# Performance work log

Hardware: AMD Instinct MI355X
Metric: run time of the kernel (lower is better)

## Reference

```python
import jax, jax.numpy as jnp
import numpy as np

# Model dims from __init__(k_mix=4, h_size=16)
H = 128            # GRU units = h_size * 8
F = 8              # per-step input features (reshape [-1,1,1,8])
KMIX = 4           # K = max(2, k_mix)
OUT = KMIX * 3     # 12; dense outputs K*3*8 = 96, reshaped to [8, 12]
T = 262144         # number of sequential bottom_generator steps


def setup_inputs() -> dict:
    key = jax.random.key(0)
    k0, k1, k2, k3 = jax.random.split(key, 4)
    even_x = jax.random.normal(k0, (T, 1, 1, F), dtype=jnp.float32)
    # GRU params (Keras layout: kernel [F, 3H], recurrent_kernel [H, 3H],
    # bias [2, 3H] for reset_after=True; gate order z, r, h)
    gru_kernel = jax.random.normal(k1, (F, 3 * H), dtype=jnp.float32) / np.float32(np.sqrt(F))
    gru_rec_kernel = jax.random.normal(k2, (H, 3 * H), dtype=jnp.float32) / np.float32(np.sqrt(H))
    gru_bias = jnp.zeros((2, 3 * H), dtype=jnp.float32)
    dense_kernel = jax.random.normal(k3, (H, F * OUT), dtype=jnp.float32) / np.float32(np.sqrt(H))
    dense_bias = jnp.zeros((F * OUT,), dtype=jnp.float32)
    return {
        "even_x": even_x,
        "gru_kernel": gru_kernel,
        "gru_rec_kernel": gru_rec_kernel,
        "gru_bias": gru_bias,
        "dense_kernel": dense_kernel,
        "dense_bias": dense_bias,
    }


def _bottom_params(even_x, gru_kernel, gru_rec_kernel, gru_bias, dense_kernel, dense_bias):
    # bottom_x = reshape(even_x, [-1, 1, 1, 8]); shift right by one with zeros
    x = even_x.reshape(-1, F)                                  # [T, 8]
    x = jnp.concatenate([jnp.zeros((1, F), x.dtype), x[:-1]], axis=0)
    b_i = gru_bias[0]
    b_r = gru_bias[1]
    # Precompute input projections for all steps (batchable part)
    gx_all = x @ gru_kernel + b_i                              # [T, 3H]

    def step(h, gx):
        gh = h @ gru_rec_kernel + b_r                          # [3H]
        xz, xr, xh = jnp.split(gx, 3)
        hz, hr, hn = jnp.split(gh, 3)
        z = jax.nn.sigmoid(xz + hz)
        r = jax.nn.sigmoid(xr + hr)
        hh = jnp.tanh(xh + r * hn)                             # reset_after=True
        h_new = z * h + (1.0 - z) * hh                         # Keras GRU update
        return h_new, h_new

    h0 = jnp.zeros((H,), x.dtype)
    _, hs = jax.lax.scan(step, h0, gx_all)                     # [T, H]
    y = hs @ dense_kernel + dense_bias                         # [T, 96]
    return y.reshape(-1, F, OUT)                               # [T, 8, 12]


def reference(even_x, gru_kernel, gru_rec_kernel, gru_bias, dense_kernel, dense_bias):
    return _bottom_params(even_x, gru_kernel, gru_rec_kernel, gru_bias,
                          dense_kernel, dense_bias)
```

## Files before the change

### kernel.cpp

```cpp
#include <hip/hip_runtime.h>
#include <hip/hip_bf16.h>
#include <stdint.h>
#include <stddef.h>

#define T_STEPS 262144
#define CHUNK   64
#define NCHUNK  (T_STEPS / CHUNK)

typedef float v2f __attribute__((ext_vector_type(2)));
typedef float v4f __attribute__((ext_vector_type(4)));

#define PKFMA(acc, a, b) \
    asm("v_pk_fma_f32 %0, %1, %2, %0" : "+v"(acc) : "v"(a), "v"(b))

__device__ __forceinline__ float dpp_xor1(float x) {
    int y = __builtin_amdgcn_mov_dpp(__builtin_bit_cast(int, x), 0xB1, 0xF, 0xF, true);
    return __builtin_bit_cast(float, y);
}
__device__ __forceinline__ float dpp_xor2(float x) {
    int y = __builtin_amdgcn_mov_dpp(__builtin_bit_cast(int, x), 0x4E, 0xF, 0xF, true);
    return __builtin_bit_cast(float, y);
}

#define FOR16(M) M(0) M(1) M(2) M(3) M(4) M(5) M(6) M(7) \
                 M(8) M(9) M(10) M(11) M(12) M(13) M(14) M(15)

__global__ __launch_bounds__(512) void gru_scan(
    const float* __restrict__ xg,
    const float* __restrict__ gk,
    const float* __restrict__ gr,
    const float* __restrict__ gb,
    __hip_bfloat16* __restrict__ hsT)
{
    const int tid = threadIdx.x;
    const int col = tid >> 2;
    const int q   = tid & 3;
    const int rq  = q << 5;

    __shared__ float hbuf[2][4][132];
    __shared__ float xsh[2][512];

#define DECLW(p) v2f wz##p, wr##p, wn##p;
    FOR16(DECLW)
#undef DECLW
#define LOADW(p) { const int r = rq + 2 * (p); \
    wz##p.x = gr[r * 384 + col];        wz##p.y = gr[(r + 1) * 384 + col]; \
    wr##p.x = gr[r * 384 + 128 + col];  wr##p.y = gr[(r + 1) * 384 + 128 + col]; \
    wn##p.x = gr[r * 384 + 256 + col];  wn##p.y = gr[(r + 1) * 384 + 256 + col]; }
    FOR16(LOADW)
#undef LOADW

    v2f kz, kr, kn;
    {
        const int f = q << 1;
        kz.x = gk[f * 384 + col];        kz.y = gk[(f + 1) * 384 + col];
        kr.x = gk[f * 384 + 128 + col];  kr.y = gk[(f + 1) * 384 + 128 + col];
        kn.x = gk[f * 384 + 256 + col];  kn.y = gk[(f + 1) * 384 + 256 + col];
    }
    const float bz  = gb[col]       + gb[384 + col];
    const float brc = gb[128 + col] + gb[512 + col];
    const float bin = gb[256 + col];
    const float brn = gb[640 + col];

    if (tid < 128) {
        hbuf[0][0][tid] = 0.0f; hbuf[0][1][tid] = 0.0f;
        hbuf[0][2][tid] = 0.0f; hbuf[0][3][tid] = 0.0f;
    }
    float hprev = 0.0f;
    float px = (tid >= 8) ? xg[tid - 8] : 0.0f;
    __syncthreads();

    for (int c = 0; c < NCHUNK; ++c) {
        const int cb = c & 1;
        xsh[cb][tid] = px;
        if (c + 1 < NCHUNK) px = xg[(c + 1) * 512 - 8 + tid];
        asm volatile("s_waitcnt lgkmcnt(0)" ::: "memory");
        __builtin_amdgcn_s_barrier();

#pragma unroll 1
        for (int s = 0; s < CHUNK; ++s) {
            const int t  = (c << 6) + s;
            const int rb = s & 1;
            const v4f* hq = (const v4f*)&hbuf[rb][q][rq];

            v2f az0 = {0.f, 0.f}, az1 = {0.f, 0.f};
            v2f ar0 = {0.f, 0.f}, ar1 = {0.f, 0.f};
            v2f an0 = {0.f, 0.f}, an1 = {0.f, 0.f};

#define QROW(m, pa, pb) { const v4f h4 = hq[m]; \
    const v2f ha = __builtin_shufflevector(h4, h4, 0, 1); \
    const v2f hb = __builtin_shufflevector(h4, h4, 2, 3); \
    PKFMA(az0, ha, wz##pa); PKFMA(az1, hb, wz##pb); \
    PKFMA(ar0, ha, wr##pa); PKFMA(ar1, hb, wr##pb); \
    PKFMA(an0, ha, wn##pa); PKFMA(an1, hb, wn##pb); }
            QROW(0, 0, 1)  QROW(1, 2, 3)   QROW(2, 4, 5)   QROW(3, 6, 7)
            QROW(4, 8, 9)  QROW(5, 10, 11) QROW(6, 12, 13) QROW(7, 14, 15)
#undef QROW

            const v2f xv = *(const v2f*)&xsh[cb][(s << 3) + (q << 1)];
            PKFMA(az0, xv, kz);
            PKFMA(ar0, xv, kr);
            v2f gx = {0.f, 0.f};
            PKFMA(gx, xv, kn);

            const v2f azs = az0 + az1;
            const v2f ars = ar0 + ar1;
            const v2f ans = an0 + an1;
            float pz  = azs.x + azs.y;
            float pr  = ars.x + ars.y;
            float pn  = ans.x + ans.y;
            float pxn = gx.x + gx.y;
            pz  += dpp_xor1(pz);  pz  += dpp_xor2(pz);
            pr  += dpp_xor1(pr);  pr  += dpp_xor2(pr);
            pn  += dpp_xor1(pn);  pn  += dpp_xor2(pn);
            pxn += dpp_xor1(pxn); pxn += dpp_xor2(pxn);

            const float zarg = pz + bz;
            const float rarg = pr + brc;
            const float hn   = pn + brn;
            const float xh   = pxn + bin;
            const float z  = 1.0f / (1.0f + __expf(-zarg));
            const float rg = 1.0f / (1.0f + __expf(-rarg));
            const float hh = 1.0f - 2.0f / (1.0f + __expf(2.0f * fmaf(rg, hn, xh)));
            const float hnew = fmaf(z, hprev - hh, hh);
            hprev = hnew;

            hbuf[rb ^ 1][q][col] = hnew;
            if (q == 1) {
                hsT[(size_t)col * T_STEPS + t] = __float2bfloat16(hnew);
            }
            asm volatile("s_waitcnt lgkmcnt(0)" ::: "memory");
            __builtin_amdgcn_s_barrier();
        }
    }
}

__global__ __launch_bounds__(256) void dense_out(
    const __hip_bfloat16* __restrict__ hsT,
    const float* __restrict__ dk,
    const float* __restrict__ db,
    float* __restrict__ out)
{
    __shared__ float wl[128 * 96];
    for (int k = threadIdx.x; k < 128 * 96; k += 256) wl[k] = dk[k];
    __syncthreads();

    const int t = blockIdx.x * 256 + threadIdx.x;
    v4f acc[24];
#pragma unroll
    for (int o = 0; o < 24; ++o) acc[o] = ((const v4f*)db)[o];

#pragma unroll 4
    for (int i = 0; i < 128; ++i) {
        const float h = __bfloat162float(hsT[(size_t)i * T_STEPS + t]);
        const v4f* wp = (const v4f*)&wl[i * 96];
#pragma unroll
        for (int o = 0; o < 24; ++o) {
            const v4f wv = wp[o];
            acc[o].x = fmaf(h, wv.x, acc[o].x);
            acc[o].y = fmaf(h, wv.y, acc[o].y);
            acc[o].z = fmaf(h, wv.z, acc[o].z);
            acc[o].w = fmaf(h, wv.w, acc[o].w);
        }
    }
    v4f* op = (v4f*)(out + (size_t)t * 96);
#pragma unroll
    for (int o = 0; o < 24; ++o) op[o] = acc[o];
}

extern "C" void kernel_launch(void* const* d_in, const int* in_sizes, int n_in,
                              void* d_out, int out_size, void* d_ws, size_t ws_size,
                              hipStream_t stream) {
    const float* even_x = (const float*)d_in[0];
    const float* gk     = (const float*)d_in[1];
    const float* gr     = (const float*)d_in[2];
    const float* gb     = (const float*)d_in[3];
    const float* dk     = (const float*)d_in[4];
    const float* db     = (const float*)d_in[5];
    float* out          = (float*)d_out;

    const size_t need = (size_t)128 * T_STEPS * sizeof(__hip_bfloat16);
    __hip_bfloat16* hsT = (ws_size >= need) ? (__hip_bfloat16*)d_ws
                                            : (__hip_bfloat16*)d_out;

    gru_scan<<<1, 512, 0, stream>>>(even_x, gk, gr, gb, hsT);
    dense_out<<<T_STEPS / 256, 256, 0, stream>>>(hsT, dk, db, out);
}
```

Before: 165.8 ms.

## Stage hidden states in LDS per chunk, use native exp2/rcp, compiler FMAs

Instead of 128 scattered 2-byte global stores per step, hidden states are kept in an LDS history buffer and written once per 64-step chunk as coalesced 16-byte vector stores. Sigmoid and tanh now use the hardware exp2 and rcp builtins instead of __expf plus a full-precision divide. The inline-asm packed FMAs are replaced with elementwise fma builtins that use one accumulator chain instead of two. Launch bounds also gain a min-blocks hint. The single accumulator makes the dependency chain longer, and the approximate rcp may cost some accuracy.

```diff
diff --git a/kernel.cpp b/kernel.cpp
--- a/kernel.cpp
+++ b/kernel.cpp
@@ -6,12 +6,11 @@
 #define T_STEPS 262144
 #define CHUNK   64
 #define NCHUNK  (T_STEPS / CHUNK)
+#define LOG2E   1.442695041f
 
 typedef float v2f __attribute__((ext_vector_type(2)));
 typedef float v4f __attribute__((ext_vector_type(4)));
-
-#define PKFMA(acc, a, b) \
-    asm("v_pk_fma_f32 %0, %1, %2, %0" : "+v"(acc) : "v"(a), "v"(b))
+typedef unsigned int v4u __attribute__((ext_vector_type(4)));
 
 __device__ __forceinline__ float dpp_xor1(float x) {
     int y = __builtin_amdgcn_mov_dpp(__builtin_bit_cast(int, x), 0xB1, 0xF, 0xF, true);
@@ -22,10 +21,13 @@
     return __builtin_bit_cast(float, y);
 }
 
+__device__ __forceinline__ float rcpf_(float x)  { return __builtin_amdgcn_rcpf(x); }
+__device__ __forceinline__ float exp2f_(float x) { return __builtin_amdgcn_exp2f(x); }
+
 #define FOR16(M) M(0) M(1) M(2) M(3) M(4) M(5) M(6) M(7) \
                  M(8) M(9) M(10) M(11) M(12) M(13) M(14) M(15)
 
-__global__ __launch_bounds__(512) void gru_scan(
+__global__ __launch_bounds__(512, 2) void gru_scan(
     const float* __restrict__ xg,
     const float* __restrict__ gk,
     const float* __restrict__ gr,
@@ -39,6 +41,7 @@
 
     __shared__ float hbuf[2][4][132];
     __shared__ float xsh[2][512];
+    __shared__ __hip_bfloat16 hist[CHUNK][128];
 
 #define DECLW(p) v2f wz##p, wr##p, wn##p;
     FOR16(DECLW)
@@ -79,36 +82,33 @@
 
 #pragma unroll 1
         for (int s = 0; s < CHUNK; ++s) {
-            const int t  = (c << 6) + s;
             const int rb = s & 1;
             const v4f* hq = (const v4f*)&hbuf[rb][q][rq];
 
-            v2f az0 = {0.f, 0.f}, az1 = {0.f, 0.f};
-            v2f ar0 = {0.f, 0.f}, ar1 = {0.f, 0.f};
-            v2f an0 = {0.f, 0.f}, an1 = {0.f, 0.f};
+            v2f az = {0.f, 0.f}, ar = {0.f, 0.f}, an = {0.f, 0.f};
 
 #define QROW(m, pa, pb) { const v4f h4 = hq[m]; \
     const v2f ha = __builtin_shufflevector(h4, h4, 0, 1); \
     const v2f hb = __builtin_shufflevector(h4, h4, 2, 3); \
-    PKFMA(az0, ha, wz##pa); PKFMA(az1, hb, wz##pb); \
-    PKFMA(ar0, ha, wr##pa); PKFMA(ar1, hb, wr##pb); \
-    PKFMA(an0, ha, wn##pa); PKFMA(an1, hb, wn##pb); }
+    az = __builtin_elementwise_fma(ha, wz##pa, az); \
+    az = __builtin_elementwise_fma(hb, wz##pb, az); \
+    ar = __builtin_elementwise_fma(ha, wr##pa, ar); \
+    ar = __builtin_elementwise_fma(hb, wr##pb, ar); \
+    an = __builtin_elementwise_fma(ha, wn##pa, an); \
+    an = __builtin_elementwise_fma(hb, wn##pb, an); }
             QROW(0, 0, 1)  QROW(1, 2, 3)   QROW(2, 4, 5)   QROW(3, 6, 7)
             QROW(4, 8, 9)  QROW(5, 10, 11) QROW(6, 12, 13) QROW(7, 14, 15)
 #undef QROW
 
             const v2f xv = *(const v2f*)&xsh[cb][(s << 3) + (q << 1)];
-            PKFMA(az0, xv, kz);
-            PKFMA(ar0, xv, kr);
+            az = __builtin_elementwise_fma(xv, kz, az);
+            ar = __builtin_elementwise_fma(xv, kr, ar);
             v2f gx = {0.f, 0.f};
-            PKFMA(gx, xv, kn);
-
-            const v2f azs = az0 + az1;
-            const v2f ars = ar0 + ar1;
-            const v2f ans = an0 + an1;
-            float pz  = azs.x + azs.y;
-            float pr  = ars.x + ars.y;
-            float pn  = ans.x + ans.y;
+            gx = __builtin_elementwise_fma(xv, kn, gx);
+
+            float pz  = az.x + az.y;
+            float pr  = ar.x + ar.y;
+            float pn  = an.x + an.y;
             float pxn = gx.x + gx.y;
             pz  += dpp_xor1(pz);  pz  += dpp_xor2(pz);
             pr  += dpp_xor1(pr);  pr  += dpp_xor2(pr);
@@ -119,18 +119,37 @@
             const float rarg = pr + brc;
             const float hn   = pn + brn;
             const float xh   = pxn + bin;
-            const float z  = 1.0f / (1.0f + __expf(-zarg));
-            const float rg = 1.0f / (1.0f + __expf(-rarg));
-            const float hh = 1.0f - 2.0f / (1.0f + __expf(2.0f * fmaf(rg, hn, xh)));
+            const float z  = rcpf_(1.0f + exp2f_(-LOG2E * zarg));
+            const float rg = rcpf_(1.0f + exp2f_(-LOG2E * rarg));
+            const float a2 = fmaf(rg, hn, xh);
+            const float hh = fmaf(-2.0f, rcpf_(1.0f + exp2f_(2.0f * LOG2E * a2)), 1.0f);
             const float hnew = fmaf(z, hprev - hh, hh);
             hprev = hnew;
 
             hbuf[rb ^ 1][q][col] = hnew;
-            if (q == 1) {
-                hsT[(size_t)col * T_STEPS + t] = __float2bfloat16(hnew);
-            }
+            if (q == 1) hist[s][col] = __float2bfloat16(hnew);
             asm volatile("s_waitcnt lgkmcnt(0)" ::: "memory");
             __builtin_amdgcn_s_barrier();
+        }
+
+        {
+            const int fc   = tid >> 2;
+            const int part = tid & 3;
+            const int sb   = part << 4;
+            unsigned int d[8];
+#pragma unroll
+            for (int j = 0; j < 8; ++j) {
+                const unsigned int lo =
+                    __builtin_bit_cast(unsigned short, hist[sb + 2 * j][fc]);
+                const unsigned int hi =
+                    __builtin_bit_cast(unsigned short, hist[sb + 2 * j + 1][fc]);
+                d[j] = lo | (hi << 16);
+            }
+            v4u* dst = (v4u*)(hsT + (size_t)fc * T_STEPS + (c << 6) + sb);
+            v4u d0; d0.x = d[0]; d0.y = d[1]; d0.z = d[2]; d0.w = d[3];
+            v4u d1; d1.x = d[4]; d1.y = d[5]; d1.z = d[6]; d1.w = d[7];
+            dst[0] = d0;
+            dst[1] = d1;
         }
     }
 }
```

Measured after the change: 140.1 ms. -15.5%, faster.
